# Kernel optimization log

Hardware: AMD Instinct MI355X
Metric: run time of the kernel (lower is better)

The kernel has to match this reference:

```python
import jax, jax.numpy as jnp
import numpy as np

N_EMBED = 1024
N_HEADS = 16
HEAD_SIZE = N_EMBED // N_HEADS
BLOCK_SIZE = 256
LN_EPS = 1e-5


def _layernorm(x, g, b):
    mu = jnp.mean(x, axis=-1, keepdims=True)
    var = jnp.var(x, axis=-1, keepdims=True)
    return (x - mu) * jax.lax.rsqrt(var + LN_EPS) * g + b


def setup_inputs() -> dict:
    key = jax.random.key(0)
    ks = jax.random.split(key, 12)
    B, T, C, H, D = 64, 256, N_EMBED, N_HEADS, HEAD_SIZE
    s = lambda fan_in: 1.0 / np.sqrt(fan_in)
    return {
        "x": jax.random.normal(ks[0], (B, T, C), jnp.float32),
        # per-head Q/K/V projections (bias=False in torch), stacked over heads
        "Wq": jax.random.uniform(ks[1], (H, C, D), jnp.float32, -s(C), s(C)),
        "Wk": jax.random.uniform(ks[2], (H, C, D), jnp.float32, -s(C), s(C)),
        "Wv": jax.random.uniform(ks[3], (H, C, D), jnp.float32, -s(C), s(C)),
        "Wproj": jax.random.uniform(ks[4], (C, C), jnp.float32, -s(C), s(C)),
        "bproj": jax.random.uniform(ks[5], (C,), jnp.float32, -s(C), s(C)),
        "W1": jax.random.uniform(ks[6], (C, 4 * C), jnp.float32, -s(C), s(C)),
        "b1": jax.random.uniform(ks[7], (4 * C,), jnp.float32, -s(C), s(C)),
        "W2": jax.random.uniform(ks[8], (4 * C, C), jnp.float32, -s(4 * C), s(4 * C)),
        "b2": jax.random.uniform(ks[9], (C,), jnp.float32, -s(4 * C), s(4 * C)),
        "ln1_g": jnp.ones((C,), jnp.float32),
        "ln1_b": jnp.zeros((C,), jnp.float32),
        "ln2_g": jnp.ones((C,), jnp.float32),
        "ln2_b": jnp.zeros((C,), jnp.float32),
    }


def reference(x, Wq, Wk, Wv, Wproj, bproj, W1, b1, W2, b2, ln1_g, ln1_b, ln2_g, ln2_b):
    B, T, C = x.shape
    # --- self-attention sub-block ---
    h = _layernorm(x, ln1_g, ln1_b)
    q = jnp.einsum("btc,hcd->bhtd", h, Wq)
    k = jnp.einsum("btc,hcd->bhtd", h, Wk)
    v = jnp.einsum("btc,hcd->bhtd", h, Wv)
    # NOTE: original scales by C**-0.5 with C = n_embed (full dim), not head_size
    scores = jnp.einsum("bhtd,bhsd->bhts", q, k) * (C ** -0.5)
    causal = jnp.tril(jnp.ones((T, T), bool))
    scores = jnp.where(causal, scores, -jnp.inf)
    wei = jax.nn.softmax(scores, axis=-1)
    attn = jnp.einsum("bhts,bhsd->bhtd", wei, v)  # [B,H,T,D]
    attn = attn.transpose(0, 2, 1, 3).reshape(B, T, C)  # concat heads
    x = x + attn @ Wproj + bproj
    # --- feed-forward sub-block ---
    h2 = _layernorm(x, ln2_g, ln2_b)
    ffn = jax.nn.relu(h2 @ W1 + b1) @ W2 + b2
    return x + ffn
```

## Files before the change

kernel.cpp:

```cpp
#include <hip/hip_runtime.h>
#include <stdint.h>

using u16 = unsigned short;
using u32 = unsigned int;

typedef __attribute__((ext_vector_type(8))) short s16x8;
typedef __attribute__((ext_vector_type(4))) float f32x4;

__device__ __forceinline__ float bflo(u32 u) { u32 t = u << 16; float f; __builtin_memcpy(&f, &t, 4); return f; }
__device__ __forceinline__ float bfhi(u32 u) { u32 t = u & 0xffff0000u; float f; __builtin_memcpy(&f, &t, 4); return f; }
__device__ __forceinline__ u16 f2bf(float f) {
  u32 u; __builtin_memcpy(&u, &f, 4);
  return (u16)((u + 0x7fffu + ((u >> 16) & 1u)) >> 16);
}

__device__ __forceinline__ void gload_lds16(const void* g, void* l) {
  __builtin_amdgcn_global_load_lds((const __attribute__((address_space(1))) void*)g,
                                   (__attribute__((address_space(3))) void*)l, 16, 0, 0);
}

__global__ __launch_bounds__(256)
void transpose_pack(const float* __restrict__ in, u16* __restrict__ out,
                    int R, int Cc, long in_bs, long out_bs)
{
  __shared__ float tile[32][33];
  in  += (size_t)blockIdx.z * in_bs;
  out += (size_t)blockIdx.z * out_bs;
  const int r0 = blockIdx.x * 32, c0 = blockIdx.y * 32;
  const int tx = threadIdx.x & 31, ty = threadIdx.x >> 5;
#pragma unroll
  for (int i = 0; i < 4; ++i) {
    int r = ty + i * 8;
    tile[r][tx] = in[(size_t)(r0 + r) * Cc + c0 + tx];
  }
  __syncthreads();
#pragma unroll
  for (int i = 0; i < 4; ++i) {
    int c = ty + i * 8;
    out[(size_t)(c0 + c) * R + r0 + tx] = f2bf(tile[tx][c]);
  }
}

__global__ __launch_bounds__(256)
void ln_f32_bf16(const float* __restrict__ x, const float* __restrict__ g,
                 const float* __restrict__ bta, u16* __restrict__ out)
{
  const int row = blockIdx.x, tid = threadIdx.x;
  const float4 v = ((const float4*)(x + (size_t)row * 1024))[tid];
  float s  = v.x + v.y + v.z + v.w;
  float ss = v.x * v.x + v.y * v.y + v.z * v.z + v.w * v.w;
#pragma unroll
  for (int m = 1; m < 64; m <<= 1) {
    s  += __shfl_xor(s, m);
    ss += __shfl_xor(ss, m);
  }
  __shared__ float red[8];
  const int wave = tid >> 6, lane = tid & 63;
  if (lane == 0) { red[wave] = s; red[4 + wave] = ss; }
  __syncthreads();
  s  = red[0] + red[1] + red[2] + red[3];
  ss = red[4] + red[5] + red[6] + red[7];
  const float mu  = s * (1.f / 1024.f);
  const float var = ss * (1.f / 1024.f) - mu * mu;
  const float rs  = rsqrtf(var + 1e-5f);
  const float4 gg = ((const float4*)g)[tid];
  const float4 bb = ((const float4*)bta)[tid];
  u32 w0 = (u32)f2bf((v.x - mu) * rs * gg.x + bb.x) | ((u32)f2bf((v.y - mu) * rs * gg.y + bb.y) << 16);
  u32 w1 = (u32)f2bf((v.z - mu) * rs * gg.z + bb.z) | ((u32)f2bf((v.w - mu) * rs * gg.w + bb.w) << 16);
  u32* outp = (u32*)(out + (size_t)row * 1024 + tid * 4);
  outp[0] = w0; outp[1] = w1;
}

template <int EPI>
__global__ __launch_bounds__(512, 2)
void gemm8p(const u16* __restrict__ A, const u16* __restrict__ B, void* __restrict__ Cv,
            const float* __restrict__ bias, const float* __restrict__ resid,
            int M, int N, int K, int GM)
{
  __shared__ u16 lds[65536];
  const int NT = K >> 6;
  const int tid = threadIdx.x;
  const int lane = tid & 63, wv = tid >> 6;
  const int wr = wv >> 2, wc = wv & 3;
  const int r = lane & 15, kg = lane >> 4;

  const int nwg = gridDim.x;
  const int q = nwg >> 3;
  const int bid = blockIdx.x;
  const int sw = (bid & 7) * q + (bid >> 3);
  const int bn = sw / GM, bm = sw % GM;

  const u16* Ab = A + (size_t)bm * 256 * K;
  const u16* Bb = B + (size_t)bn * 256 * K;

  const u32 ldsb = (u32)(uintptr_t)lds;
  const u32 segb = (u32)((kg ^ (r >> 1)) << 4);
  const u32 abase = ldsb + (u32)((wr * 128 + r) * 128) + segb;
  const u32 bbase = ldsb + 65536u + (u32)((wc * 64 + r) * 128) + segb;

  f32x4 acc[8][4];
#pragma unroll
  for (int m = 0; m < 8; ++m)
#pragma unroll
    for (int n = 0; n < 4; ++n) acc[m][n] = f32x4{0.f, 0.f, 0.f, 0.f};

  auto stage = [&](const u16* src, int u, int h, int base_u16) {
#pragma unroll
    for (int jj = 0; jj < 2; ++jj) {
      int ci = jj * 512 + tid;
      int rl = ci >> 3;
      int sseg = (ci & 7) ^ ((rl >> 1) & 7);
      gload_lds16(src + (size_t)(h * 128 + rl) * K + u * 64 + sseg * 8,
                  &lds[base_u16 + h * 8192 + ci * 8]);
    }
  };

#define DSR(d, a, o) asm volatile("ds_read_b128 %0, %1 offset:" o : "=v"(d) : "v"(a))
#define ISSUE12(aR, bR) \
  DSR(bv0, bR, "0"); DSR(bv1, bR, "2048"); DSR(bv2, bR, "4096"); DSR(bv3, bR, "6144"); \
  DSR(av0, aR, "0"); DSR(av1, aR, "2048"); DSR(av2, aR, "4096"); DSR(av3, aR, "6144"); \
  DSR(av4, aR, "8192"); DSR(av5, aR, "10240"); DSR(av6, aR, "12288"); DSR(av7, aR, "14336")
#define MM(m, n) acc[m][n] = __builtin_amdgcn_mfma_f32_16x16x32_bf16(av##m, bv##n, acc[m][n], 0, 0, 0)
#define RUNG(m, cnt) \
  asm volatile("s_waitcnt lgkmcnt(" #cnt ")" ::: "memory"); \
  __builtin_amdgcn_sched_barrier(0); \
  MM(m, 0); MM(m, 1); MM(m, 2); MM(m, 3)
#define LADDER() \
  RUNG(0, 7); RUNG(1, 6); RUNG(2, 5); RUNG(3, 4); \
  RUNG(4, 3); RUNG(5, 2); RUNG(6, 1); RUNG(7, 0)

  stage(Ab, 0, 0, 0);      stage(Ab, 0, 1, 0);
  stage(Bb, 0, 0, 32768);  stage(Bb, 0, 1, 32768);
  asm volatile("s_waitcnt vmcnt(0)" ::: "memory");
  __builtin_amdgcn_s_barrier();

  for (int t = 0; t < NT; ++t) {
    const int buf = t & 1;
    const bool s1 = (t + 1) < NT;
    const int nb = (buf ^ 1) * 16384;
    const u32 aA0 = abase + (u32)(buf * 32768);
    const u32 aB0 = bbase + (u32)(buf * 32768);
    const u32 aA1 = aA0 ^ 64u;
    const u32 aB1 = aB0 ^ 64u;

    if (s1) {
      stage(Ab, t + 1, 0, nb);           stage(Ab, t + 1, 1, nb);
      stage(Bb, t + 1, 0, 32768 + nb);   stage(Bb, t + 1, 1, 32768 + nb);
    }
    __builtin_amdgcn_sched_barrier(0);
    __builtin_amdgcn_s_setprio(1);
    {
      s16x8 av0, av1, av2, av3, av4, av5, av6, av7, bv0, bv1, bv2, bv3;
      ISSUE12(aA0, aB0);
      LADDER();
    }
    {
      s16x8 av0, av1, av2, av3, av4, av5, av6, av7, bv0, bv1, bv2, bv3;
      ISSUE12(aA1, aB1);
      LADDER();
    }
    __builtin_amdgcn_s_setprio(0);
    __builtin_amdgcn_sched_barrier(0);
    asm volatile("s_waitcnt vmcnt(0)" ::: "memory");
    __builtin_amdgcn_s_barrier();
  }

#pragma unroll
  for (int m = 0; m < 8; ++m) {
#pragma unroll
    for (int n = 0; n < 4; ++n) {
#pragma unroll
      for (int j = 0; j < 4; ++j) {
        int row = bm * 256 + wr * 128 + m * 16 + kg * 4 + j;
        int col = bn * 256 + wc * 64 + n * 16 + r;
        size_t idx = (size_t)row * N + col;
        float v = acc[m][n][j];
        if constexpr (EPI == 0) {
          ((u16*)Cv)[idx] = f2bf(v);
        } else if constexpr (EPI == 1) {
          ((float*)Cv)[idx] = v + bias[col] + resid[idx];
        } else if constexpr (EPI == 2) {
          ((u16*)Cv)[idx] = f2bf(fmaxf(v + bias[col], 0.f));
        } else {
          ((float*)Cv)[idx] = v + bias[col] + resid[idx];
        }
      }
    }
  }
#undef DSR
#undef ISSUE12
#undef MM
#undef RUNG
#undef LADDER
}

__global__ __launch_bounds__(256)
void attn_mfma(const u16* __restrict__ qkv, u16* __restrict__ outc)
{
  const int bh = blockIdx.x, b = bh >> 4, h = bh & 15;
  const int tid = threadIdx.x;
  const int lane = tid & 63, w = tid >> 6;
  const int r = lane & 15, kg = lane >> 4;

  __shared__ u16 Ks[64 * 64];
  __shared__ u16 Vt[64 * 72];
  __shared__ u16 P[4][64 * 72];

  const u16* qbase = qkv + (size_t)(b * 256) * 3072 + h * 64;

  s16x8 qf[4][2];
#pragma unroll
  for (int m = 0; m < 4; ++m)
#pragma unroll
    for (int ks = 0; ks < 2; ++ks)
      qf[m][ks] = *(const s16x8*)(qbase + (size_t)(w * 64 + m * 16 + r) * 3072 + ks * 32 + kg * 8);

  f32x4 of[4][4];
  float mrun[4][4], lrun[4][4];
#pragma unroll
  for (int m = 0; m < 4; ++m) {
#pragma unroll
    for (int n = 0; n < 4; ++n) of[m][n] = f32x4{0.f, 0.f, 0.f, 0.f};
#pragma unroll
    for (int j = 0; j < 4; ++j) { mrun[m][j] = -1e30f; lrun[m][j] = 0.f; }
  }

  const float cexp = 0.03125f * 1.4426950408889634f;

  for (int kt = 0; kt < 4; ++kt) {
#pragma unroll
    for (int jj = 0; jj < 2; ++jj) {
      int ci = jj * 256 + tid;
      int key = ci >> 3, seg = ci & 7;
      int sseg = seg ^ (key & 7);
      gload_lds16(qkv + (size_t)(b * 256 + kt * 64 + key) * 3072 + 1024 + h * 64 + sseg * 8,
                  &Ks[ci * 8]);
    }
    {
      int row = tid >> 2, q = tid & 3;
      const u16* vg = qkv + (size_t)(b * 256 + kt * 64 + row) * 3072 + 2048 + h * 64 + q * 16;
      union { uint4 u[2]; u16 s[16]; } vv;
      vv.u[0] = *(const uint4*)vg;
      vv.u[1] = *(const uint4*)(vg + 8);
#pragma unroll
      for (int i = 0; i < 16; ++i)
        Vt[(q * 16 + i) * 72 + row] = vv.s[i];
    }
    __syncthreads();

    if (w >= kt) {
      f32x4 s[4][4];
#pragma unroll
      for (int m = 0; m < 4; ++m)
#pragma unroll
        for (int n = 0; n < 4; ++n) s[m][n] = f32x4{0.f, 0.f, 0.f, 0.f};
#pragma unroll
      for (int ks = 0; ks < 2; ++ks) {
        s16x8 kb[4];
#pragma unroll
        for (int n = 0; n < 4; ++n) {
          int row = n * 16 + r;
          int sseg = (ks * 4 + kg) ^ (row & 7);
          kb[n] = *(const s16x8*)&Ks[row * 64 + sseg * 8];
        }
#pragma unroll
        for (int m = 0; m < 4; ++m)
#pragma unroll
          for (int n = 0; n < 4; ++n)
            s[m][n] = __builtin_amdgcn_mfma_f32_16x16x32_bf16(qf[m][ks], kb[n], s[m][n], 0, 0, 0);
      }
      if (kt == w) {
#pragma unroll
        for (int m = 0; m < 4; ++m)
#pragma unroll
          for (int n = 0; n < 4; ++n)
#pragma unroll
            for (int j = 0; j < 4; ++j)
              if (n * 16 + r > m * 16 + kg * 4 + j) s[m][n][j] = -1e30f;
      }
#pragma unroll
      for (int m = 0; m < 4; ++m) {
        float rm[4], rsc[4], ls[4];
#pragma unroll
        for (int j = 0; j < 4; ++j) {
          rm[j] = fmaxf(fmaxf(s[m][0][j], s[m][1][j]), fmaxf(s[m][2][j], s[m][3][j]));
          rm[j] = fmaxf(rm[j], __shfl_xor(rm[j], 1));
          rm[j] = fmaxf(rm[j], __shfl_xor(rm[j], 2));
          rm[j] = fmaxf(rm[j], __shfl_xor(rm[j], 4));
          rm[j] = fmaxf(rm[j], __shfl_xor(rm[j], 8));
          float mnew = fmaxf(mrun[m][j], rm[j]);
          rsc[j] = exp2f((mrun[m][j] - mnew) * cexp);
          mrun[m][j] = mnew;
          ls[j] = 0.f;
        }
#pragma unroll
        for (int n = 0; n < 4; ++n)
#pragma unroll
          for (int j = 0; j < 4; ++j) {
            float p = exp2f((s[m][n][j] - mrun[m][j]) * cexp);
            ls[j] += p;
            P[w][(m * 16 + kg * 4 + j) * 72 + n * 16 + r] = f2bf(p);
          }
#pragma unroll
        for (int j = 0; j < 4; ++j) {
          ls[j] += __shfl_xor(ls[j], 1);
          ls[j] += __shfl_xor(ls[j], 2);
          ls[j] += __shfl_xor(ls[j], 4);
          ls[j] += __shfl_xor(ls[j], 8);
          lrun[m][j] = lrun[m][j] * rsc[j] + ls[j];
        }
#pragma unroll
        for (int n = 0; n < 4; ++n)
#pragma unroll
          for (int j = 0; j < 4; ++j)
            of[m][n][j] *= rsc[j];
      }
#pragma unroll
      for (int kk = 0; kk < 2; ++kk) {
        s16x8 pa[4], vb[4];
#pragma unroll
        for (int m = 0; m < 4; ++m)
          pa[m] = *(const s16x8*)&P[w][(m * 16 + r) * 72 + kk * 32 + kg * 8];
#pragma unroll
        for (int n = 0; n < 4; ++n)
          vb[n] = *(const s16x8*)&Vt[(n * 16 + r) * 72 + kk * 32 + kg * 8];
#pragma unroll
        for (int m = 0; m < 4; ++m)
#pragma unroll
          for (int n = 0; n < 4; ++n)
            of[m][n] = __builtin_amdgcn_mfma_f32_16x16x32_bf16(pa[m], vb[n], of[m][n], 0, 0, 0);
      }
    }
    __syncthreads();
  }

#pragma unroll
  for (int m = 0; m < 4; ++m) {
    float inv[4];
#pragma unroll
    for (int j = 0; j < 4; ++j) inv[j] = 1.f / lrun[m][j];
#pragma unroll
    for (int n = 0; n < 4; ++n)
#pragma unroll
      for (int j = 0; j < 4; ++j) {
        int row = b * 256 + w * 64 + m * 16 + kg * 4 + j;
        outc[(size_t)row * 1024 + h * 64 + n * 16 + r] = f2bf(of[m][n][j] * inv[j]);
      }
  }
}

extern "C" void kernel_launch(void* const* d_in, const int* in_sizes, int n_in,
                              void* d_out, int out_size, void* d_ws, size_t ws_size,
                              hipStream_t stream) {
  (void)in_sizes; (void)n_in; (void)out_size; (void)ws_size;
  const float* x     = (const float*)d_in[0];
  const float* Wq    = (const float*)d_in[1];
  const float* Wk    = (const float*)d_in[2];
  const float* Wv    = (const float*)d_in[3];
  const float* Wproj = (const float*)d_in[4];
  const float* bproj = (const float*)d_in[5];
  const float* W1    = (const float*)d_in[6];
  const float* b1    = (const float*)d_in[7];
  const float* W2    = (const float*)d_in[8];
  const float* b2    = (const float*)d_in[9];
  const float* ln1g  = (const float*)d_in[10];
  const float* ln1b  = (const float*)d_in[11];
  const float* ln2g  = (const float*)d_in[12];
  const float* ln2b  = (const float*)d_in[13];
  float* out = (float*)d_out;

  char* ws = (char*)d_ws;
  u16*   WqkvT  = (u16*)(ws + 0);
  u16*   WprojT = (u16*)(ws + 6291456);
  u16*   W1T    = (u16*)(ws + 8388608);
  u16*   W2T    = (u16*)(ws + 16777216);
  u16*   hb     = (u16*)(ws + 25165824);
  u16*   qkvb   = (u16*)(ws + 58720256);
  float* x2     = (float*)(ws + 159383552);
  u16*   h2     = (u16*)(ws + 226492416);
  u16*   ffn1   = (u16*)(ws + 25165824);
  u16*   attnout = hb;

  const int M = 16384;

  transpose_pack<<<dim3(32, 2, 16), 256, 0, stream>>>(Wq, WqkvT,           1024, 64, 65536, 65536);
  transpose_pack<<<dim3(32, 2, 16), 256, 0, stream>>>(Wk, WqkvT + 1048576, 1024, 64, 65536, 65536);
  transpose_pack<<<dim3(32, 2, 16), 256, 0, stream>>>(Wv, WqkvT + 2097152, 1024, 64, 65536, 65536);
  transpose_pack<<<dim3(32, 32, 1), 256, 0, stream>>>(Wproj, WprojT, 1024, 1024, 0, 0);
  transpose_pack<<<dim3(32, 128, 1), 256, 0, stream>>>(W1, W1T, 1024, 4096, 0, 0);
  transpose_pack<<<dim3(128, 32, 1), 256, 0, stream>>>(W2, W2T, 4096, 1024, 0, 0);

  ln_f32_bf16<<<M, 256, 0, stream>>>(x, ln1g, ln1b, hb);

  gemm8p<0><<<64 * 12, 512, 0, stream>>>(hb, WqkvT, qkvb, nullptr, nullptr, M, 3072, 1024, 64);

  attn_mfma<<<1024, 256, 0, stream>>>(qkvb, attnout);

  gemm8p<1><<<64 * 4, 512, 0, stream>>>(attnout, WprojT, x2, bproj, x, M, 1024, 1024, 64);

  ln_f32_bf16<<<M, 256, 0, stream>>>(x2, ln2g, ln2b, h2);

  gemm8p<2><<<64 * 16, 512, 0, stream>>>(h2, W1T, ffn1, b1, nullptr, M, 4096, 1024, 64);

  gemm8p<3><<<64 * 4, 512, 0, stream>>>(ffn1, W2T, out, b2, x2, M, 1024, 4096, 64);
}
```

Baseline: 619.0 us.

## Store residual x2 in bf16 and remap GEMM tiles per XCD

The intermediate residual x2 is now written as bf16 instead of fp32. This halves the bytes for the proj-GEMM output, the LN2 input and the FFN2 residual read. The GEMM block-to-tile mapping is also replaced with a per-XCD rectangular assignment (CM/CN/XN), so each XCD works on a compact tile region for better L2 reuse. The cost is bf16 rounding on the residual path, which lowers accuracy of the final output.

```diff
diff --git a/kernel.cpp b/kernel.cpp
--- a/kernel.cpp
+++ b/kernel.cpp
@@ -7,8 +7,7 @@
 typedef __attribute__((ext_vector_type(8))) short s16x8;
 typedef __attribute__((ext_vector_type(4))) float f32x4;
 
-__device__ __forceinline__ float bflo(u32 u) { u32 t = u << 16; float f; __builtin_memcpy(&f, &t, 4); return f; }
-__device__ __forceinline__ float bfhi(u32 u) { u32 t = u & 0xffff0000u; float f; __builtin_memcpy(&f, &t, 4); return f; }
+__device__ __forceinline__ float bf2f(u16 u) { u32 t = (u32)u << 16; float f; __builtin_memcpy(&f, &t, 4); return f; }
 __device__ __forceinline__ u16 f2bf(float f) {
   u32 u; __builtin_memcpy(&u, &f, 4);
   return (u16)((u + 0x7fffu + ((u >> 16) & 1u)) >> 16);
@@ -41,12 +40,20 @@
   }
 }
 
+template <int IN>
 __global__ __launch_bounds__(256)
-void ln_f32_bf16(const float* __restrict__ x, const float* __restrict__ g,
-                 const float* __restrict__ bta, u16* __restrict__ out)
+void ln_to_bf16(const void* __restrict__ xv, const float* __restrict__ g,
+                const float* __restrict__ bta, u16* __restrict__ out)
 {
   const int row = blockIdx.x, tid = threadIdx.x;
-  const float4 v = ((const float4*)(x + (size_t)row * 1024))[tid];
+  float4 v;
+  if constexpr (IN == 0) {
+    v = ((const float4*)((const float*)xv + (size_t)row * 1024))[tid];
+  } else {
+    uint2 u = ((const uint2*)((const u16*)xv + (size_t)row * 1024))[tid];
+    v.x = bf2f((u16)(u.x & 0xffff)); v.y = bf2f((u16)(u.x >> 16));
+    v.z = bf2f((u16)(u.y & 0xffff)); v.w = bf2f((u16)(u.y >> 16));
+  }
   float s  = v.x + v.y + v.z + v.w;
   float ss = v.x * v.x + v.y * v.y + v.z * v.z + v.w * v.w;
 #pragma unroll
@@ -74,8 +81,8 @@
 template <int EPI>
 __global__ __launch_bounds__(512, 2)
 void gemm8p(const u16* __restrict__ A, const u16* __restrict__ B, void* __restrict__ Cv,
-            const float* __restrict__ bias, const float* __restrict__ resid,
-            int M, int N, int K, int GM)
+            const float* __restrict__ bias, const void* __restrict__ resid,
+            int M, int N, int K, int CM, int CN, int XN)
 {
   __shared__ u16 lds[65536];
   const int NT = K >> 6;
@@ -84,11 +91,10 @@
   const int wr = wv >> 2, wc = wv & 3;
   const int r = lane & 15, kg = lane >> 4;
 
-  const int nwg = gridDim.x;
-  const int q = nwg >> 3;
   const int bid = blockIdx.x;
-  const int sw = (bid & 7) * q + (bid >> 3);
-  const int bn = sw / GM, bm = sw % GM;
+  const int x = bid & 7, i = bid >> 3;
+  const int bm = (x / XN) * CM + i / CN;
+  const int bn = (x % XN) * CN + i % CN;
 
   const u16* Ab = A + (size_t)bm * 256 * K;
   const u16* Bb = B + (size_t)bn * 256 * K;
@@ -178,11 +184,11 @@
         if constexpr (EPI == 0) {
           ((u16*)Cv)[idx] = f2bf(v);
         } else if constexpr (EPI == 1) {
-          ((float*)Cv)[idx] = v + bias[col] + resid[idx];
+          ((u16*)Cv)[idx] = f2bf(v + bias[col] + ((const float*)resid)[idx]);
         } else if constexpr (EPI == 2) {
           ((u16*)Cv)[idx] = f2bf(fmaxf(v + bias[col], 0.f));
         } else {
-          ((float*)Cv)[idx] = v + bias[col] + resid[idx];
+          ((float*)Cv)[idx] = v + bias[col] + bf2f(((const u16*)resid)[idx]);
         }
       }
     }
@@ -376,7 +382,7 @@
   u16*   W2T    = (u16*)(ws + 16777216);
   u16*   hb     = (u16*)(ws + 25165824);
   u16*   qkvb   = (u16*)(ws + 58720256);
-  float* x2     = (float*)(ws + 159383552);
+  u16*   x2     = (u16*)(ws + 159383552);
   u16*   h2     = (u16*)(ws + 226492416);
   u16*   ffn1   = (u16*)(ws + 25165824);
   u16*   attnout = hb;
@@ -390,17 +396,17 @@
   transpose_pack<<<dim3(32, 128, 1), 256, 0, stream>>>(W1, W1T, 1024, 4096, 0, 0);
   transpose_pack<<<dim3(128, 32, 1), 256, 0, stream>>>(W2, W2T, 4096, 1024, 0, 0);
 
-  ln_f32_bf16<<<M, 256, 0, stream>>>(x, ln1g, ln1b, hb);
-
-  gemm8p<0><<<64 * 12, 512, 0, stream>>>(hb, WqkvT, qkvb, nullptr, nullptr, M, 3072, 1024, 64);
+  ln_to_bf16<0><<<M, 256, 0, stream>>>(x, ln1g, ln1b, hb);
+
+  gemm8p<0><<<768, 512, 0, stream>>>(hb, WqkvT, qkvb, nullptr, nullptr, M, 3072, 1024, 16, 6, 2);
 
   attn_mfma<<<1024, 256, 0, stream>>>(qkvb, attnout);
 
-  gemm8p<1><<<64 * 4, 512, 0, stream>>>(attnout, WprojT, x2, bproj, x, M, 1024, 1024, 64);
-
-  ln_f32_bf16<<<M, 256, 0, stream>>>(x2, ln2g, ln2b, h2);
-
-  gemm8p<2><<<64 * 16, 512, 0, stream>>>(h2, W1T, ffn1, b1, nullptr, M, 4096, 1024, 64);
-
-  gemm8p<3><<<64 * 4, 512, 0, stream>>>(ffn1, W2T, out, b2, x2, M, 1024, 4096, 64);
-}
+  gemm8p<1><<<256, 512, 0, stream>>>(attnout, WprojT, x2, bproj, x, M, 1024, 1024, 8, 4, 1);
+
+  ln_to_bf16<1><<<M, 256, 0, stream>>>(x2, ln2g, ln2b, h2);
+
+  gemm8p<2><<<1024, 512, 0, stream>>>(h2, W1T, ffn1, b1, nullptr, M, 4096, 1024, 16, 8, 2);
+
+  gemm8p<3><<<256, 512, 0, stream>>>(ffn1, W2T, out, b2, x2, M, 1024, 4096, 8, 4, 1);
+}
```

New measurement: 557.1 us. 1.11x faster.
